# Performance work log

Hardware: AMD Instinct MI355X
Metric: run time of the kernel (lower is better)

## Reference

```python
import jax, jax.numpy as jnp
import numpy as np

EMB = 64   # embedding_dim
OUT = 64   # out_channels (== EMB so conv layers stack)
EF = 16    # num_edge_features
L = 2      # num_layers
NC, NT = 5000, 10000
E, EL = 50000, 20000


def setup_inputs():
    key = jax.random.key(0)
    it = iter(jax.random.split(key, 40))
    def nrm(shape, s=0.05):
        return jax.random.normal(next(it), shape, dtype=jnp.float32) * s
    def ri(n, hi):
        return jax.random.randint(next(it), (n,), 0, hi, dtype=jnp.int32)
    return dict(
        x_c=jnp.arange(NC, dtype=jnp.int32),
        x_t=jnp.arange(NT, dtype=jnp.int32),
        edge_src_ct=ri(E, NC), edge_dst_ct=ri(E, NT),
        edge_src_tc=ri(E, NT), edge_dst_tc=ri(E, NC),
        edge_label_src=ri(EL, NC), edge_label_dst=ri(EL, NT),
        edge_attr_ct=nrm((E, EF), 1.0),
        edge_attr_tc=nrm((E, EF), 1.0),
        edge_label_attr=nrm((EL, EF), 1.0),
        emb_c=nrm((NC, EMB), 1.0), emb_t=nrm((NT, EMB), 1.0),
        ntl_c_w=nrm((EMB, EMB)), ntl_c_b=nrm((EMB,)),
        ntl_t_w=nrm((EMB, EMB)), ntl_t_b=nrm((EMB,)),
        conv_mlp1_w=nrm((L, 2, EF, OUT)), conv_mlp1_b=nrm((L, 2, OUT)),
        conv_mlp2_w=nrm((L, 2, OUT, EMB * OUT)), conv_mlp2_b=nrm((L, 2, EMB * OUT)),
        conv_root_w=nrm((L, 2, EMB, OUT)), conv_root_b=nrm((L, 2, OUT)),
        ph_w0=nrm((2 * EMB + EF, 64)), ph_b0=nrm((64,)),
        ph_w1=nrm((64, 64)), ph_b1=nrm((64,)),
        ph_w2=nrm((64, 1)), ph_b2=nrm((1,)),
    )


def _nnconv(h_src, h_dst, src, dst, eattr, m1w, m1b, m2w, m2b, rw, rb, n_dst):
    # edge-conditioned weight matrices: [E, EMB, OUT]
    W = (jax.nn.relu(eattr @ m1w + m1b) @ m2w + m2b).reshape(-1, EMB, OUT)
    msg = jnp.einsum('ei,eio->eo', h_src[src], W)        # gather + per-edge matmul
    agg = jax.ops.segment_max(msg, dst, num_segments=n_dst)
    agg = jnp.where(jnp.isneginf(agg), 0.0, agg)         # isolated nodes -> 0 (PyG semantics)
    return agg + h_dst @ rw + rb                          # root weight + bias


def reference(x_c, x_t, edge_src_ct, edge_dst_ct, edge_src_tc, edge_dst_tc,
              edge_label_src, edge_label_dst, edge_attr_ct, edge_attr_tc,
              edge_label_attr, emb_c, emb_t, ntl_c_w, ntl_c_b, ntl_t_w, ntl_t_b,
              conv_mlp1_w, conv_mlp1_b, conv_mlp2_w, conv_mlp2_b,
              conv_root_w, conv_root_b, ph_w0, ph_b0, ph_w1, ph_b1, ph_w2, ph_b2):
    h_c = emb_c[x_c] @ ntl_c_w + ntl_c_b
    h_t = emb_t[x_t] @ ntl_t_w + ntl_t_b
    for l in range(L):
        new_t = _nnconv(h_c, h_t, edge_src_ct, edge_dst_ct, edge_attr_ct,
                        conv_mlp1_w[l, 0], conv_mlp1_b[l, 0], conv_mlp2_w[l, 0],
                        conv_mlp2_b[l, 0], conv_root_w[l, 0], conv_root_b[l, 0], NT)
        new_c = _nnconv(h_t, h_c, edge_src_tc, edge_dst_tc, edge_attr_tc,
                        conv_mlp1_w[l, 1], conv_mlp1_b[l, 1], conv_mlp2_w[l, 1],
                        conv_mlp2_b[l, 1], conv_root_w[l, 1], conv_root_b[l, 1], NC)
        h_c, h_t = jax.nn.relu(new_c), jax.nn.relu(new_t)
    z = jnp.concatenate([h_c[edge_label_src], h_t[edge_label_dst], edge_label_attr], axis=-1)
    z = jax.nn.relu(z @ ph_w0 + ph_b0)
    z = jax.nn.relu(z @ ph_w1 + ph_b1)
    logits = z @ ph_w2 + ph_b2
    preds = jax.nn.sigmoid(logits).squeeze()
    return preds, logits
```

## Files before the change

### kernel.cpp

```cpp
#include <hip/hip_runtime.h>
#include <hip/hip_bf16.h>
#include <math.h>

#define NCN   5000
#define NTN   10000
#define NEDGE 50000
#define NLBL  20000
#define EBLK  196

typedef _Float16 f16x8 __attribute__((ext_vector_type(8)));
typedef _Float16 f16x4 __attribute__((ext_vector_type(4)));
typedef float    f32x4 __attribute__((ext_vector_type(4)));

#define HSTRIDE 264
#define NSLICE  130
#define ZSTR    72

__device__ __forceinline__ void atomicMaxF(float* addr, float v) {
  if (v >= 0.0f) atomicMax((int*)addr, __float_as_int(v));
  else           atomicMin((unsigned int*)addr, __float_as_uint(v));
}

__device__ __forceinline__ void stage16(const _Float16* g, _Float16* l) {
  __builtin_amdgcn_global_load_lds(
      (const __attribute__((address_space(1))) void*)g,
      (__attribute__((address_space(3))) void*)l, 16, 0, 0);
}

__global__ __launch_bounds__(256) void fill_neginf(float* __restrict__ p, int n) {
  int i = blockIdx.x * 256 + threadIdx.x;
  if (i < n) p[i] = -INFINITY;
}

__global__ __launch_bounds__(256) void prep_B(
    const float* __restrict__ m2w, const float* __restrict__ m2b,
    _Float16* __restrict__ out)
{
  int p = blockIdx.x / NSLICE;
  int s = blockIdx.x % NSLICE;
  int t = threadIdx.x;
  int hi = t >> 6, col = t & 63;
  const float* w  = m2w + p * 64 * 4096;
  const float* bb = m2b + p * 4096;
  f16x8 v;
  #pragma unroll
  for (int j = 0; j < 8; ++j) {
    float x;
    if (s < 128) {
      int h = s >> 1, i = (s & 1) * 32 + hi * 8 + j;
      x = w[h * 4096 + i * 64 + col];
    } else {
      int i = (s - 128) * 32 + hi * 8 + j;
      x = bb[i * 64 + col];
    }
    v[j] = (_Float16)x;
  }
  *(f16x8*)(out + ((size_t)(p * NSLICE + s)) * 2048 + t * 8) = v;
}

__global__ __launch_bounds__(256) void prep_m1(
    const float* __restrict__ m1w, const float* __restrict__ m1b,
    _Float16* __restrict__ out)
{
  int p = blockIdx.x;
  int t = threadIdx.x;
  int hi = t >> 6, col = t & 63;
  f16x8 v;
  #pragma unroll
  for (int j = 0; j < 8; ++j) {
    int i = hi * 8 + j;
    float x = (i < 16) ? m1w[p * 1024 + i * 64 + col]
            : (i == 16) ? m1b[p * 64 + col] : 0.0f;
    v[j] = (_Float16)x;
  }
  *(f16x8*)(out + (size_t)p * 2048 + t * 8) = v;
}

__global__ __launch_bounds__(256) void prep_headB(
    const float* __restrict__ w0, const float* __restrict__ b0,
    const float* __restrict__ w1, const float* __restrict__ b1,
    _Float16* __restrict__ out)
{
  int s = blockIdx.x;
  int t = threadIdx.x;
  int hi = t >> 6, col = t & 63;
  f16x8 v;
  #pragma unroll
  for (int j = 0; j < 8; ++j) {
    int k = hi * 8 + j;
    float x = 0.0f;
    if (s < 5) {
      int kr = s * 32 + k;
      x = (kr < 144) ? w0[kr * 64 + col] : (kr == 144 ? b0[col] : 0.0f);
    } else {
      int kr = (s - 5) * 32 + k;
      x = (kr < 64) ? w1[kr * 64 + col] : (kr == 64 ? b1[col] : 0.0f);
    }
    v[j] = (_Float16)x;
  }
  *(f16x8*)(out + (size_t)s * 2048 + t * 8) = v;
}

struct NtArgs {
  const float* emb0; const int* idx0; const float* w0; const float* b0; float* out0; int n0; int blk0;
  const float* emb1; const int* idx1; const float* w1; const float* b1; float* out1; int n1;
};

__global__ __launch_bounds__(256) void node_transform2(NtArgs a) {
  int bid = blockIdx.x;
  int dir = (bid >= a.blk0) ? 1 : 0;
  int lb  = bid - (dir ? a.blk0 : 0);
  const float* emb = dir ? a.emb1 : a.emb0;
  const int*   idx = dir ? a.idx1 : a.idx0;
  const float* w   = dir ? a.w1   : a.w0;
  const float* b   = dir ? a.b1   : a.b0;
  float*       out = dir ? a.out1 : a.out0;
  int          n   = dir ? a.n1   : a.n0;

  __shared__ float s_w[64 * 64];
  __shared__ float s_b[64];
  int tid = threadIdx.x;
  for (int i = tid; i < 4096; i += 256) s_w[i] = w[i];
  if (tid < 64) s_b[tid] = b[tid];
  __syncthreads();
  int wave = tid >> 6, lane = tid & 63;
  int node = lb * 4 + wave;
  if (node >= n) return;
  float v = emb[idx[node] * 64 + lane];
  float acc = s_b[lane];
  #pragma unroll 8
  for (int i = 0; i < 64; ++i)
    acc = fmaf(__shfl(v, i, 64), s_w[i * 64 + lane], acc);
  out[node * 64 + lane] = acc;
}

struct ConvArgs {
  const float* h_src0; const int* esrc0; const int* edst0; const float* ea0;
  const _Float16* B0; const _Float16* m10; float* agg0;
  const float* h_src1; const int* esrc1; const int* edst1; const float* ea1;
  const _Float16* B1; const _Float16* m11; float* agg1;
};

__global__ __launch_bounds__(256) void conv_msg_mfma2(ConvArgs a) {
  __shared__ __align__(16) _Float16 s_B[2][4][2048];
  __shared__ __align__(16) _Float16 s_m1f[2048];
  __shared__ __align__(16) _Float16 s_hidT[64 * HSTRIDE];
  __shared__ int s_srcn[256];
  __shared__ int s_dst[256];

  const int bid = blockIdx.x;
  const int dir = (bid >= EBLK) ? 1 : 0;
  const int eb  = bid - (dir ? EBLK : 0);

  const float*    h_src  = dir ? a.h_src1 : a.h_src0;
  const int*      esrc   = dir ? a.esrc1  : a.esrc0;
  const int*      edst   = dir ? a.edst1  : a.edst0;
  const float*    eattr  = dir ? a.ea1    : a.ea0;
  const _Float16* Bready = dir ? a.B1     : a.B0;
  const _Float16* m1rdy  = dir ? a.m11    : a.m10;
  float*          agg    = dir ? a.agg1   : a.agg0;

  const int tid  = threadIdx.x;
  const int e0   = eb * 256;
  const int w    = tid >> 6;
  const int lane = tid & 63;
  const int l15  = lane & 15;
  const int hi   = lane >> 4;
  const int w64  = w * 64;

  stage16(m1rdy + tid * 8, &s_m1f[tid * 8]);
  #pragma unroll
  for (int q = 0; q < 4; ++q)
    stage16(Bready + (size_t)q * 2048 + tid * 8, &s_B[0][q][tid * 8]);

  {
    int ge = e0 + tid;
    s_srcn[tid] = (ge < NEDGE) ? esrc[ge] : 0;
    s_dst[tid]  = (ge < NEDGE) ? edst[ge] : -1;
  }
  __syncthreads();

  f16x8 hv0[4], hv1[4];
  #pragma unroll
  for (int m = 0; m < 4; ++m) {
    int el = w64 + m * 16 + l15;
    const float* src = h_src + (size_t)s_srcn[el] * 64;
    float4 a0 = *(const float4*)(src + hi * 8);
    float4 a1 = *(const float4*)(src + hi * 8 + 4);
    float4 b0 = *(const float4*)(src + 32 + hi * 8);
    float4 b1 = *(const float4*)(src + 32 + hi * 8 + 4);
    hv0[m] = (f16x8){(_Float16)a0.x,(_Float16)a0.y,(_Float16)a0.z,(_Float16)a0.w,
                     (_Float16)a1.x,(_Float16)a1.y,(_Float16)a1.z,(_Float16)a1.w};
    hv1[m] = (f16x8){(_Float16)b0.x,(_Float16)b0.y,(_Float16)b0.z,(_Float16)b0.w,
                     (_Float16)b1.x,(_Float16)b1.y,(_Float16)b1.z,(_Float16)b1.w};
  }

  {
    f16x8 ea[4];
    #pragma unroll
    for (int m = 0; m < 4; ++m) {
      int ge = e0 + w64 + m * 16 + l15;
      f16x8 v = {};
      if (hi < 2) {
        if (ge < NEDGE) {
          float4 f0 = *(const float4*)(eattr + (size_t)ge * 16 + hi * 8);
          float4 f1 = *(const float4*)(eattr + (size_t)ge * 16 + hi * 8 + 4);
          v = (f16x8){(_Float16)f0.x,(_Float16)f0.y,(_Float16)f0.z,(_Float16)f0.w,
                      (_Float16)f1.x,(_Float16)f1.y,(_Float16)f1.z,(_Float16)f1.w};
        }
      } else if (hi == 2) {
        v[0] = (_Float16)1.0f;
      }
      ea[m] = v;
    }
    f32x4 hacc[4][4] = {};
    #pragma unroll
    for (int n = 0; n < 4; ++n) {
      f16x8 bm = *(const f16x8*)&s_m1f[(hi * 64 + n * 16 + l15) * 8];
      #pragma unroll
      for (int m = 0; m < 4; ++m)
        hacc[m][n] = __builtin_amdgcn_mfma_f32_16x16x32_f16(ea[m], bm, hacc[m][n], 0, 0, 0);
    }
    #pragma unroll
    for (int m = 0; m < 4; ++m) {
      #pragma unroll
      for (int n = 0; n < 4; ++n) {
        int h  = n * 16 + l15;
        int e4 = w64 + m * 16 + hi * 4;
        f16x4 hval;
        #pragma unroll
        for (int r = 0; r < 4; ++r) hval[r] = (_Float16)fmaxf(hacc[m][n][r], 0.0f);
        *(f16x4*)&s_hidT[h * HSTRIDE + e4] = hval;
      }
    }
  }

  f32x4 acc[4][4] = {};

#define MFMA_SLICE(P_, SS, HV, HH)                                            \
  {                                                                           \
    f16x8 b0 = *(const f16x8*)&s_B[P_][SS][(hi * 64 +  0 + l15) * 8];         \
    f16x8 b1 = *(const f16x8*)&s_B[P_][SS][(hi * 64 + 16 + l15) * 8];         \
    f16x8 b2 = *(const f16x8*)&s_B[P_][SS][(hi * 64 + 32 + l15) * 8];         \
    f16x8 b3 = *(const f16x8*)&s_B[P_][SS][(hi * 64 + 48 + l15) * 8];         \
    _Pragma("unroll")                                                         \
    for (int m = 0; m < 4; ++m) {                                             \
      f16x8 av = (f16x8)(HV[m] * HH[m]);                                      \
      acc[m][0] = __builtin_amdgcn_mfma_f32_16x16x32_f16(av, b0, acc[m][0], 0, 0, 0); \
      acc[m][1] = __builtin_amdgcn_mfma_f32_16x16x32_f16(av, b1, acc[m][1], 0, 0, 0); \
      acc[m][2] = __builtin_amdgcn_mfma_f32_16x16x32_f16(av, b2, acc[m][2], 0, 0, 0); \
      acc[m][3] = __builtin_amdgcn_mfma_f32_16x16x32_f16(av, b3, acc[m][3], 0, 0, 0); \
    }                                                                         \
  }

#define BIAS_SLICE(P_, SS, HV)                                                \
  {                                                                           \
    f16x8 b0 = *(const f16x8*)&s_B[P_][SS][(hi * 64 +  0 + l15) * 8];         \
    f16x8 b1 = *(const f16x8*)&s_B[P_][SS][(hi * 64 + 16 + l15) * 8];         \
    f16x8 b2 = *(const f16x8*)&s_B[P_][SS][(hi * 64 + 32 + l15) * 8];         \
    f16x8 b3 = *(const f16x8*)&s_B[P_][SS][(hi * 64 + 48 + l15) * 8];         \
    _Pragma("unroll")                                                         \
    for (int m = 0; m < 4; ++m) {                                             \
      f16x8 av = HV[m];                                                       \
      acc[m][0] = __builtin_amdgcn_mfma_f32_16x16x32_f16(av, b0, acc[m][0], 0, 0, 0); \
      acc[m][1] = __builtin_amdgcn_mfma_f32_16x16x32_f16(av, b1, acc[m][1], 0, 0, 0); \
      acc[m][2] = __builtin_amdgcn_mfma_f32_16x16x32_f16(av, b2, acc[m][2], 0, 0, 0); \
      acc[m][3] = __builtin_amdgcn_mfma_f32_16x16x32_f16(av, b3, acc[m][3], 0, 0, 0); \
    }                                                                         \
  }

  for (int p = 0; p < 33; ++p) {
    const int P = p & 1;
    if (p < 31) {
      #pragma unroll
      for (int q = 0; q < 4; ++q)
        stage16(Bready + (size_t)(4 * p + 4 + q) * 2048 + tid * 8,
                &s_B[P ^ 1][q][tid * 8]);
    } else if (p == 31) {
      stage16(Bready + (size_t)128 * 2048 + tid * 8, &s_B[P ^ 1][0][tid * 8]);
      stage16(Bready + (size_t)129 * 2048 + tid * 8, &s_B[P ^ 1][1][tid * 8]);
    }
    if (p < 32) {
      _Float16 hA[4], hB[4];
      #pragma unroll
      for (int m = 0; m < 4; ++m)
        hA[m] = s_hidT[(2 * p) * HSTRIDE + w64 + m * 16 + l15];
      #pragma unroll
      for (int m = 0; m < 4; ++m)
        hB[m] = s_hidT[(2 * p + 1) * HSTRIDE + w64 + m * 16 + l15];
      MFMA_SLICE(P, 0, hv0, hA);
      MFMA_SLICE(P, 1, hv1, hA);
      MFMA_SLICE(P, 2, hv0, hB);
      MFMA_SLICE(P, 3, hv1, hB);
    } else {
      BIAS_SLICE(P, 0, hv0);
      BIAS_SLICE(P, 1, hv1);
    }
    asm volatile("s_waitcnt vmcnt(0)" ::: "memory");
    __builtin_amdgcn_s_barrier();
  }
#undef MFMA_SLICE
#undef BIAS_SLICE

  #pragma unroll
  for (int m = 0; m < 4; ++m) {
    int d0 = s_dst[w64 + m * 16 + hi * 4 + 0];
    int d1 = s_dst[w64 + m * 16 + hi * 4 + 1];
    int d2 = s_dst[w64 + m * 16 + hi * 4 + 2];
    int d3 = s_dst[w64 + m * 16 + hi * 4 + 3];
    #pragma unroll
    for (int n = 0; n < 4; ++n) {
      int o = n * 16 + l15;
      if (d0 >= 0) atomicMaxF(&agg[(size_t)d0 * 64 + o], acc[m][n][0]);
      if (d1 >= 0) atomicMaxF(&agg[(size_t)d1 * 64 + o], acc[m][n][1]);
      if (d2 >= 0) atomicMaxF(&agg[(size_t)d2 * 64 + o], acc[m][n][2]);
      if (d3 >= 0) atomicMaxF(&agg[(size_t)d3 * 64 + o], acc[m][n][3]);
    }
  }
}

struct FinArgs {
  float* agg0; const float* hold0; const float* rw0; const float* rb0; float* hnew0; int n0; int blk0;
  float* agg1; const float* hold1; const float* rw1; const float* rb1; float* hnew1; int n1;
};

__global__ __launch_bounds__(256) void conv_finalize2(FinArgs a) {
  int bid = blockIdx.x;
  int dir = (bid >= a.blk0) ? 1 : 0;
  int lb  = bid - (dir ? a.blk0 : 0);
  float*       agg  = dir ? a.agg1  : a.agg0;
  const float* hold = dir ? a.hold1 : a.hold0;
  const float* rw   = dir ? a.rw1   : a.rw0;
  const float* rb   = dir ? a.rb1   : a.rb0;
  float*       hnew = dir ? a.hnew1 : a.hnew0;
  int          n    = dir ? a.n1    : a.n0;

  __shared__ float s_w[64 * 64];
  __shared__ float s_b[64];
  int tid = threadIdx.x;
  for (int i = tid; i < 4096; i += 256) s_w[i] = rw[i];
  if (tid < 64) s_b[tid] = rb[tid];
  __syncthreads();
  int wave = tid >> 6, lane = tid & 63;
  int node = lb * 4 + wave;
  if (node >= n) return;
  float v = hold[node * 64 + lane];
  float acc = s_b[lane];
  #pragma unroll 8
  for (int i = 0; i < 64; ++i)
    acc = fmaf(__shfl(v, i, 64), s_w[i * 64 + lane], acc);
  float va = agg[node * 64 + lane];
  agg[node * 64 + lane] = -INFINITY;
  if (va == -INFINITY) va = 0.0f;
  hnew[node * 64 + lane] = fmaxf(va + acc, 0.0f);
}

__global__ __launch_bounds__(256) void head_mfma(
    const float* __restrict__ h_c, const float* __restrict__ h_t,
    const int* __restrict__ lsrc, const int* __restrict__ ldst,
    const float* __restrict__ lattr,
    const _Float16* __restrict__ headB,
    const float* __restrict__ w2, const float* __restrict__ b2,
    float* __restrict__ preds, float* __restrict__ logits, int nL)
{
  __shared__ __align__(16) _Float16 s_W[8][2048];
  __shared__ __align__(16) _Float16 s_z[4][32][ZSTR];
  __shared__ float s_w2[64];

  const int tid = threadIdx.x;
  const int wv = tid >> 6, lane = tid & 63;
  const int l15 = lane & 15, hi = lane >> 4;

  #pragma unroll
  for (int s = 0; s < 8; ++s)
    stage16(headB + s * 2048 + tid * 8, &s_W[s][tid * 8]);
  if (tid < 64) s_w2[tid] = w2[tid];
  const float b2v = b2[0];

  const int e0 = blockIdx.x * 128 + wv * 32;

  f16x8 ac[2][2], at[2][2], aa[2];
  #pragma unroll
  for (int m = 0; m < 2; ++m) {
    int e = e0 + m * 16 + l15;
    int ee = (e < nL) ? e : 0;
    const float* pc = h_c + (size_t)lsrc[ee] * 64;
    const float* pt = h_t + (size_t)ldst[ee] * 64;
    #pragma unroll
    for (int half = 0; half < 2; ++half) {
      float4 c0 = *(const float4*)(pc + half * 32 + hi * 8);
      float4 c1 = *(const float4*)(pc + half * 32 + hi * 8 + 4);
      float4 t0 = *(const float4*)(pt + half * 32 + hi * 8);
      float4 t1 = *(const float4*)(pt + half * 32 + hi * 8 + 4);
      ac[m][half] = (f16x8){(_Float16)c0.x,(_Float16)c0.y,(_Float16)c0.z,(_Float16)c0.w,
                            (_Float16)c1.x,(_Float16)c1.y,(_Float16)c1.z,(_Float16)c1.w};
      at[m][half] = (f16x8){(_Float16)t0.x,(_Float16)t0.y,(_Float16)t0.z,(_Float16)t0.w,
                            (_Float16)t1.x,(_Float16)t1.y,(_Float16)t1.z,(_Float16)t1.w};
    }
    f16x8 v = {};
    if (hi < 2) {
      float4 f0 = *(const float4*)(lattr + (size_t)ee * 16 + hi * 8);
      float4 f1 = *(const float4*)(lattr + (size_t)ee * 16 + hi * 8 + 4);
      v = (f16x8){(_Float16)f0.x,(_Float16)f0.y,(_Float16)f0.z,(_Float16)f0.w,
                  (_Float16)f1.x,(_Float16)f1.y,(_Float16)f1.z,(_Float16)f1.w};
    } else if (hi == 2) {
      v[0] = (_Float16)1.0f;
    }
    aa[m] = v;
  }

  __syncthreads();

  f32x4 acc1[2][4] = {};
  #pragma unroll
  for (int s = 0; s < 5; ++s) {
    f16x8 bfr[4];
    #pragma unroll
    for (int nn = 0; nn < 4; ++nn)
      bfr[nn] = *(const f16x8*)&s_W[s][(hi * 64 + nn * 16 + l15) * 8];
    #pragma unroll
    for (int m = 0; m < 2; ++m) {
      f16x8 a = (s == 0) ? ac[m][0] : (s == 1) ? ac[m][1]
              : (s == 2) ? at[m][0] : (s == 3) ? at[m][1] : aa[m];
      #pragma unroll
      for (int nn = 0; nn < 4; ++nn)
        acc1[m][nn] = __builtin_amdgcn_mfma_f32_16x16x32_f16(a, bfr[nn], acc1[m][nn], 0, 0, 0);
    }
  }

  #pragma unroll
  for (int m = 0; m < 2; ++m)
    #pragma unroll
    for (int nn = 0; nn < 4; ++nn)
      #pragma unroll
      for (int r = 0; r < 4; ++r)
        s_z[wv][m * 16 + hi * 4 + r][nn * 16 + l15] =
            (_Float16)fmaxf(acc1[m][nn][r], 0.0f);

  f16x8 abias = {};
  if (hi == 0) abias[0] = (_Float16)1.0f;
  f32x4 acc2[2][4] = {};
  #pragma unroll
  for (int s = 0; s < 3; ++s) {
    f16x8 bfr[4];
    #pragma unroll
    for (int nn = 0; nn < 4; ++nn)
      bfr[nn] = *(const f16x8*)&s_W[5 + s][(hi * 64 + nn * 16 + l15) * 8];
    #pragma unroll
    for (int m = 0; m < 2; ++m) {
      f16x8 a = (s < 2) ? *(const f16x8*)&s_z[wv][m * 16 + l15][s * 32 + hi * 8] : abias;
      #pragma unroll
      for (int nn = 0; nn < 4; ++nn)
        acc2[m][nn] = __builtin_amdgcn_mfma_f32_16x16x32_f16(a, bfr[nn], acc2[m][nn], 0, 0, 0);
    }
  }

  #pragma unroll
  for (int m = 0; m < 2; ++m) {
    float part[4];
    #pragma unroll
    for (int r = 0; r < 4; ++r) {
      float p = 0.0f;
      #pragma unroll
      for (int nn = 0; nn < 4; ++nn)
        p = fmaf(fmaxf(acc2[m][nn][r], 0.0f), s_w2[nn * 16 + l15], p);
      part[r] = p;
    }
    #pragma unroll
    for (int off = 1; off < 16; off <<= 1) {
      #pragma unroll
      for (int r = 0; r < 4; ++r)
        part[r] += __shfl_xor(part[r], off, 64);
    }
    if (l15 == 0) {
      #pragma unroll
      for (int r = 0; r < 4; ++r) {
        int e = e0 + m * 16 + hi * 4 + r;
        if (e < nL) {
          float lg = part[r] + b2v;
          logits[e] = lg;
          preds[e]  = 1.0f / (1.0f + expf(-lg));
        }
      }
    }
  }
}

extern "C" void kernel_launch(void* const* d_in, const int* in_sizes, int n_in,
                              void* d_out, int out_size, void* d_ws, size_t ws_size,
                              hipStream_t stream) {
  const int*   x_c      = (const int*)  d_in[0];
  const int*   x_t      = (const int*)  d_in[1];
  const int*   esrc_ct  = (const int*)  d_in[2];
  const int*   edst_ct  = (const int*)  d_in[3];
  const int*   esrc_tc  = (const int*)  d_in[4];
  const int*   edst_tc  = (const int*)  d_in[5];
  const int*   lbl_src  = (const int*)  d_in[6];
  const int*   lbl_dst  = (const int*)  d_in[7];
  const float* eattr_ct = (const float*)d_in[8];
  const float* eattr_tc = (const float*)d_in[9];
  const float* lbl_attr = (const float*)d_in[10];
  const float* emb_c    = (const float*)d_in[11];
  const float* emb_t    = (const float*)d_in[12];
  const float* ntl_c_w  = (const float*)d_in[13];
  const float* ntl_c_b  = (const float*)d_in[14];
  const float* ntl_t_w  = (const float*)d_in[15];
  const float* ntl_t_b  = (const float*)d_in[16];
  const float* m1w      = (const float*)d_in[17];
  const float* m1b      = (const float*)d_in[18];
  const float* m2w      = (const float*)d_in[19];
  const float* m2b      = (const float*)d_in[20];
  const float* rw       = (const float*)d_in[21];
  const float* rb       = (const float*)d_in[22];
  const float* ph_w0    = (const float*)d_in[23];
  const float* ph_b0    = (const float*)d_in[24];
  const float* ph_w1    = (const float*)d_in[25];
  const float* ph_b1    = (const float*)d_in[26];
  const float* ph_w2    = (const float*)d_in[27];
  const float* ph_b2    = (const float*)d_in[28];

  float* out = (float*)d_out;

  float* ws = (float*)d_ws;
  float* h_c0  = ws;
  float* h_c1  = h_c0 + NCN * 64;
  float* h_t0  = h_c1 + NCN * 64;
  float* h_t1  = h_t0 + NTN * 64;
  float* agg_c = h_t1 + NTN * 64;
  float* agg_t = agg_c + NCN * 64;
  _Float16* Bready  = (_Float16*)(agg_t + NTN * 64);
  _Float16* m1ready = Bready + 4 * NSLICE * 2048;
  _Float16* headBr  = m1ready + 4 * 2048;

  prep_B    <<<4 * NSLICE, 256, 0, stream>>>(m2w, m2b, Bready);
  prep_m1   <<<4, 256, 0, stream>>>(m1w, m1b, m1ready);
  prep_headB<<<8, 256, 0, stream>>>(ph_w0, ph_b0, ph_w1, ph_b1, headBr);

  {
    NtArgs na;
    na.emb0 = emb_c; na.idx0 = x_c; na.w0 = ntl_c_w; na.b0 = ntl_c_b; na.out0 = h_c0; na.n0 = NCN;
    na.blk0 = (NCN + 3) / 4;
    na.emb1 = emb_t; na.idx1 = x_t; na.w1 = ntl_t_w; na.b1 = ntl_t_b; na.out1 = h_t0; na.n1 = NTN;
    node_transform2<<<(NCN + 3) / 4 + (NTN + 3) / 4, 256, 0, stream>>>(na);
  }

  fill_neginf<<<((NCN + NTN) * 64 + 255) / 256, 256, 0, stream>>>(agg_c, (NCN + NTN) * 64);

  float* hc_cur = h_c0; float* hc_nxt = h_c1;
  float* ht_cur = h_t0; float* ht_nxt = h_t1;

  for (int l = 0; l < 2; ++l) {
    int p0 = l * 2 + 0;
    int p1 = l * 2 + 1;
    {
      ConvArgs ca;
      ca.h_src0 = hc_cur; ca.esrc0 = esrc_ct; ca.edst0 = edst_ct; ca.ea0 = eattr_ct;
      ca.B0 = Bready + (size_t)p0 * NSLICE * 2048; ca.m10 = m1ready + (size_t)p0 * 2048;
      ca.agg0 = agg_t;
      ca.h_src1 = ht_cur; ca.esrc1 = esrc_tc; ca.edst1 = edst_tc; ca.ea1 = eattr_tc;
      ca.B1 = Bready + (size_t)p1 * NSLICE * 2048; ca.m11 = m1ready + (size_t)p1 * 2048;
      ca.agg1 = agg_c;
      conv_msg_mfma2<<<2 * EBLK, 256, 0, stream>>>(ca);
    }
    {
      FinArgs fa;
      fa.agg0 = agg_t; fa.hold0 = ht_cur; fa.rw0 = rw + p0 * 4096; fa.rb0 = rb + p0 * 64;
      fa.hnew0 = ht_nxt; fa.n0 = NTN; fa.blk0 = (NTN + 3) / 4;
      fa.agg1 = agg_c; fa.hold1 = hc_cur; fa.rw1 = rw + p1 * 4096; fa.rb1 = rb + p1 * 64;
      fa.hnew1 = hc_nxt; fa.n1 = NCN;
      conv_finalize2<<<(NTN + 3) / 4 + (NCN + 3) / 4, 256, 0, stream>>>(fa);
    }
    float* t;
    t = hc_cur; hc_cur = hc_nxt; hc_nxt = t;
    t = ht_cur; ht_cur = ht_nxt; ht_nxt = t;
  }

  head_mfma<<<(NLBL + 127) / 128, 256, 0, stream>>>(
      hc_cur, ht_cur, lbl_src, lbl_dst, lbl_attr,
      headBr, ph_w2, ph_b2,
      out, out + NLBL, NLBL);
}
```

Measured before the change: 249.6 us.

## Replace atomic segment-max with CSR-sorted edges and deterministic segment reduction

Builds a per-destination CSR (count, scan, scatter) each call, processes edges in destination-sorted order, writes per-edge messages to a dense buffer, and computes the segment max in the finalize kernel instead of with float atomics. This removes 64 scattered atomics per edge and the -inf fill kernel. In exchange it adds three preprocessing kernels, a memset, a single-block scan per direction, and a large message write and read-back through memory (about 25 MB per layer). Padding slots past 50000 read perm entries zeroed by the memset, so they gather edge 0 and write unused rows.

```diff
diff --git a/kernel.cpp b/kernel.cpp
--- a/kernel.cpp
+++ b/kernel.cpp
@@ -5,6 +5,7 @@
 #define NCN   5000
 #define NTN   10000
 #define NEDGE 50000
+#define ESLOT 50176
 #define NLBL  20000
 #define EBLK  196
 
@@ -15,21 +16,11 @@
 #define HSTRIDE 264
 #define NSLICE  130
 #define ZSTR    72
-
-__device__ __forceinline__ void atomicMaxF(float* addr, float v) {
-  if (v >= 0.0f) atomicMax((int*)addr, __float_as_int(v));
-  else           atomicMin((unsigned int*)addr, __float_as_uint(v));
-}
 
 __device__ __forceinline__ void stage16(const _Float16* g, _Float16* l) {
   __builtin_amdgcn_global_load_lds(
       (const __attribute__((address_space(1))) void*)g,
       (__attribute__((address_space(3))) void*)l, 16, 0, 0);
-}
-
-__global__ __launch_bounds__(256) void fill_neginf(float* __restrict__ p, int n) {
-  int i = blockIdx.x * 256 + threadIdx.x;
-  if (i < n) p[i] = -INFINITY;
 }
 
 __global__ __launch_bounds__(256) void prep_B(
@@ -99,6 +90,65 @@
     v[j] = (_Float16)x;
   }
   *(f16x8*)(out + (size_t)s * 2048 + t * 8) = v;
+}
+
+__global__ __launch_bounds__(256) void count_edges(
+    const int* __restrict__ dT, const int* __restrict__ dC,
+    int* __restrict__ cT, int* __restrict__ cC)
+{
+  int i = blockIdx.x * 256 + threadIdx.x;
+  if (i < NEDGE) atomicAdd(&cT[dT[i]], 1);
+  else { int j = i - NEDGE; if (j < NEDGE) atomicAdd(&cC[dC[j]], 1); }
+}
+
+struct ScanArgs { const int* c0; int* o0; int n0; const int* c1; int* o1; int n1; };
+
+__global__ __launch_bounds__(1024) void scan2(ScanArgs a) {
+  const int* c = blockIdx.x ? a.c1 : a.c0;
+  int*       o = blockIdx.x ? a.o1 : a.o0;
+  int        n = blockIdx.x ? a.n1 : a.n0;
+  __shared__ int lds[1024];
+  int t = threadIdx.x;
+  int CH = (n + 1023) / 1024;
+  int base = t * CH;
+  int s = 0;
+  for (int i = 0; i < CH; ++i) { int idx = base + i; if (idx < n) s += c[idx]; }
+  lds[t] = s;
+  __syncthreads();
+  #pragma unroll
+  for (int d = 1; d < 1024; d <<= 1) {
+    int v = (t >= d) ? lds[t - d] : 0;
+    __syncthreads();
+    lds[t] += v;
+    __syncthreads();
+  }
+  int run = lds[t] - s;
+  for (int i = 0; i < CH; ++i) {
+    int idx = base + i;
+    if (idx < n) { o[idx] = run; run += c[idx]; }
+  }
+  if (t == 1023) o[n] = lds[1023];
+}
+
+__global__ __launch_bounds__(256) void scatter_edges(
+    const int* __restrict__ dT, const int* __restrict__ dC,
+    const int* __restrict__ oT, const int* __restrict__ oC,
+    int* __restrict__ curT, int* __restrict__ curC,
+    int* __restrict__ permT, int* __restrict__ permC)
+{
+  int i = blockIdx.x * 256 + threadIdx.x;
+  if (i < NEDGE) {
+    int d = dT[i];
+    int p = atomicAdd(&curT[d], 1);
+    permT[oT[d] + p] = i;
+  } else {
+    int j = i - NEDGE;
+    if (j < NEDGE) {
+      int d = dC[j];
+      int p = atomicAdd(&curC[d], 1);
+      permC[oC[d] + p] = j;
+    }
+  }
 }
 
 struct NtArgs {
@@ -135,10 +185,10 @@
 }
 
 struct ConvArgs {
-  const float* h_src0; const int* esrc0; const int* edst0; const float* ea0;
-  const _Float16* B0; const _Float16* m10; float* agg0;
-  const float* h_src1; const int* esrc1; const int* edst1; const float* ea1;
-  const _Float16* B1; const _Float16* m11; float* agg1;
+  const float* h_src0; const int* esrc0; const float* ea0;
+  const int* perm0; const _Float16* B0; const _Float16* m10; float* msg0;
+  const float* h_src1; const int* esrc1; const float* ea1;
+  const int* perm1; const _Float16* B1; const _Float16* m11; float* msg1;
 };
 
 __global__ __launch_bounds__(256) void conv_msg_mfma2(ConvArgs a) {
@@ -146,7 +196,7 @@
   __shared__ __align__(16) _Float16 s_m1f[2048];
   __shared__ __align__(16) _Float16 s_hidT[64 * HSTRIDE];
   __shared__ int s_srcn[256];
-  __shared__ int s_dst[256];
+  __shared__ int s_eidx[256];
 
   const int bid = blockIdx.x;
   const int dir = (bid >= EBLK) ? 1 : 0;
@@ -154,11 +204,11 @@
 
   const float*    h_src  = dir ? a.h_src1 : a.h_src0;
   const int*      esrc   = dir ? a.esrc1  : a.esrc0;
-  const int*      edst   = dir ? a.edst1  : a.edst0;
   const float*    eattr  = dir ? a.ea1    : a.ea0;
+  const int*      eperm  = dir ? a.perm1  : a.perm0;
   const _Float16* Bready = dir ? a.B1     : a.B0;
   const _Float16* m1rdy  = dir ? a.m11    : a.m10;
-  float*          agg    = dir ? a.agg1   : a.agg0;
+  float*          msg    = dir ? a.msg1   : a.msg0;
 
   const int tid  = threadIdx.x;
   const int e0   = eb * 256;
@@ -174,9 +224,9 @@
     stage16(Bready + (size_t)q * 2048 + tid * 8, &s_B[0][q][tid * 8]);
 
   {
-    int ge = e0 + tid;
-    s_srcn[tid] = (ge < NEDGE) ? esrc[ge] : 0;
-    s_dst[tid]  = (ge < NEDGE) ? edst[ge] : -1;
+    int e = eperm[e0 + tid];
+    s_eidx[tid] = e;
+    s_srcn[tid] = esrc[e];
   }
   __syncthreads();
 
@@ -199,15 +249,14 @@
     f16x8 ea[4];
     #pragma unroll
     for (int m = 0; m < 4; ++m) {
-      int ge = e0 + w64 + m * 16 + l15;
+      int li = w64 + m * 16 + l15;
+      int e  = s_eidx[li];
       f16x8 v = {};
       if (hi < 2) {
-        if (ge < NEDGE) {
-          float4 f0 = *(const float4*)(eattr + (size_t)ge * 16 + hi * 8);
-          float4 f1 = *(const float4*)(eattr + (size_t)ge * 16 + hi * 8 + 4);
-          v = (f16x8){(_Float16)f0.x,(_Float16)f0.y,(_Float16)f0.z,(_Float16)f0.w,
-                      (_Float16)f1.x,(_Float16)f1.y,(_Float16)f1.z,(_Float16)f1.w};
-        }
+        float4 f0 = *(const float4*)(eattr + (size_t)e * 16 + hi * 8);
+        float4 f1 = *(const float4*)(eattr + (size_t)e * 16 + hi * 8 + 4);
+        v = (f16x8){(_Float16)f0.x,(_Float16)f0.y,(_Float16)f0.z,(_Float16)f0.w,
+                    (_Float16)f1.x,(_Float16)f1.y,(_Float16)f1.z,(_Float16)f1.w};
       } else if (hi == 2) {
         v[0] = (_Float16)1.0f;
       }
@@ -304,31 +353,30 @@
 
   #pragma unroll
   for (int m = 0; m < 4; ++m) {
-    int d0 = s_dst[w64 + m * 16 + hi * 4 + 0];
-    int d1 = s_dst[w64 + m * 16 + hi * 4 + 1];
-    int d2 = s_dst[w64 + m * 16 + hi * 4 + 2];
-    int d3 = s_dst[w64 + m * 16 + hi * 4 + 3];
-    #pragma unroll
-    for (int n = 0; n < 4; ++n) {
-      int o = n * 16 + l15;
-      if (d0 >= 0) atomicMaxF(&agg[(size_t)d0 * 64 + o], acc[m][n][0]);
-      if (d1 >= 0) atomicMaxF(&agg[(size_t)d1 * 64 + o], acc[m][n][1]);
-      if (d2 >= 0) atomicMaxF(&agg[(size_t)d2 * 64 + o], acc[m][n][2]);
-      if (d3 >= 0) atomicMaxF(&agg[(size_t)d3 * 64 + o], acc[m][n][3]);
-    }
-  }
-}
-
-struct FinArgs {
-  float* agg0; const float* hold0; const float* rw0; const float* rb0; float* hnew0; int n0; int blk0;
-  float* agg1; const float* hold1; const float* rw1; const float* rb1; float* hnew1; int n1;
+    #pragma unroll
+    for (int r = 0; r < 4; ++r) {
+      int sl = e0 + w64 + m * 16 + hi * 4 + r;
+      float* row = msg + (size_t)sl * 64;
+      #pragma unroll
+      for (int n = 0; n < 4; ++n)
+        row[n * 16 + l15] = acc[m][n][r];
+    }
+  }
+}
+
+struct SegArgs {
+  const float* msg0; const int* off0; const float* hold0; const float* rw0; const float* rb0;
+  float* hnew0; int n0; int blk0;
+  const float* msg1; const int* off1; const float* hold1; const float* rw1; const float* rb1;
+  float* hnew1; int n1;
 };
 
-__global__ __launch_bounds__(256) void conv_finalize2(FinArgs a) {
+__global__ __launch_bounds__(256) void segfin2(SegArgs a) {
   int bid = blockIdx.x;
   int dir = (bid >= a.blk0) ? 1 : 0;
   int lb  = bid - (dir ? a.blk0 : 0);
-  float*       agg  = dir ? a.agg1  : a.agg0;
+  const float* msg  = dir ? a.msg1  : a.msg0;
+  const int*   off  = dir ? a.off1  : a.off0;
   const float* hold = dir ? a.hold1 : a.hold0;
   const float* rw   = dir ? a.rw1   : a.rw0;
   const float* rb   = dir ? a.rb1   : a.rb0;
@@ -344,15 +392,19 @@
   int wave = tid >> 6, lane = tid & 63;
   int node = lb * 4 + wave;
   if (node >= n) return;
+
+  int k0 = off[node], k1 = off[node + 1];
+  float mx = -INFINITY;
+  for (int k = k0; k < k1; ++k)
+    mx = fmaxf(mx, msg[(size_t)k * 64 + lane]);
+  if (k0 == k1) mx = 0.0f;
+
   float v = hold[node * 64 + lane];
   float acc = s_b[lane];
   #pragma unroll 8
   for (int i = 0; i < 64; ++i)
     acc = fmaf(__shfl(v, i, 64), s_w[i * 64 + lane], acc);
-  float va = agg[node * 64 + lane];
-  agg[node * 64 + lane] = -INFINITY;
-  if (va == -INFINITY) va = 0.0f;
-  hnew[node * 64 + lane] = fmaxf(va + acc, 0.0f);
+  hnew[node * 64 + lane] = fmaxf(mx + acc, 0.0f);
 }
 
 __global__ __launch_bounds__(256) void head_mfma(
@@ -522,15 +574,35 @@
   float* out = (float*)d_out;
 
   float* ws = (float*)d_ws;
-  float* h_c0  = ws;
-  float* h_c1  = h_c0 + NCN * 64;
-  float* h_t0  = h_c1 + NCN * 64;
-  float* h_t1  = h_t0 + NTN * 64;
-  float* agg_c = h_t1 + NTN * 64;
-  float* agg_t = agg_c + NCN * 64;
-  _Float16* Bready  = (_Float16*)(agg_t + NTN * 64);
+  float* h_c0 = ws;
+  float* h_c1 = h_c0 + NCN * 64;
+  float* h_t0 = h_c1 + NCN * 64;
+  float* h_t1 = h_t0 + NTN * 64;
+  float* msgT = h_t1 + NTN * 64;
+  float* msgC = msgT + (size_t)ESLOT * 64;
+  _Float16* Bready  = (_Float16*)(msgC + (size_t)ESLOT * 64);
   _Float16* m1ready = Bready + 4 * NSLICE * 2048;
   _Float16* headBr  = m1ready + 4 * 2048;
+  int* ip     = (int*)(headBr + 8 * 2048);
+  int* offT   = ip;               ip += NTN + 1;
+  int* offC   = ip;               ip += NCN + 1;
+  int* cntT   = ip;               ip += NTN;
+  int* cntC   = ip;               ip += NCN;
+  int* curT   = ip;               ip += NTN;
+  int* curC   = ip;               ip += NCN;
+  int* permT  = ip;               ip += ESLOT;
+  int* permC  = ip;               ip += ESLOT;
+  size_t zero_bytes = (size_t)(2 * (NTN + NCN) + 2 * ESLOT) * sizeof(int);
+
+  hipMemsetAsync(cntT, 0, zero_bytes, stream);
+  count_edges<<<(2 * NEDGE + 255) / 256, 256, 0, stream>>>(edst_ct, edst_tc, cntT, cntC);
+  {
+    ScanArgs sa; sa.c0 = cntT; sa.o0 = offT; sa.n0 = NTN;
+    sa.c1 = cntC; sa.o1 = offC; sa.n1 = NCN;
+    scan2<<<2, 1024, 0, stream>>>(sa);
+  }
+  scatter_edges<<<(2 * NEDGE + 255) / 256, 256, 0, stream>>>(
+      edst_ct, edst_tc, offT, offC, curT, curC, permT, permC);
 
   prep_B    <<<4 * NSLICE, 256, 0, stream>>>(m2w, m2b, Bready);
   prep_m1   <<<4, 256, 0, stream>>>(m1w, m1b, m1ready);
@@ -544,8 +616,6 @@
     node_transform2<<<(NCN + 3) / 4 + (NTN + 3) / 4, 256, 0, stream>>>(na);
   }
 
-  fill_neginf<<<((NCN + NTN) * 64 + 255) / 256, 256, 0, stream>>>(agg_c, (NCN + NTN) * 64);
-
   float* hc_cur = h_c0; float* hc_nxt = h_c1;
   float* ht_cur = h_t0; float* ht_nxt = h_t1;
 
@@ -554,21 +624,23 @@
     int p1 = l * 2 + 1;
     {
       ConvArgs ca;
-      ca.h_src0 = hc_cur; ca.esrc0 = esrc_ct; ca.edst0 = edst_ct; ca.ea0 = eattr_ct;
+      ca.h_src0 = hc_cur; ca.esrc0 = esrc_ct; ca.ea0 = eattr_ct; ca.perm0 = permT;
       ca.B0 = Bready + (size_t)p0 * NSLICE * 2048; ca.m10 = m1ready + (size_t)p0 * 2048;
-      ca.agg0 = agg_t;
-      ca.h_src1 = ht_cur; ca.esrc1 = esrc_tc; ca.edst1 = edst_tc; ca.ea1 = eattr_tc;
+      ca.msg0 = msgT;
+      ca.h_src1 = ht_cur; ca.esrc1 = esrc_tc; ca.ea1 = eattr_tc; ca.perm1 = permC;
       ca.B1 = Bready + (size_t)p1 * NSLICE * 2048; ca.m11 = m1ready + (size_t)p1 * 2048;
-      ca.agg1 = agg_c;
+      ca.msg1 = msgC;
       conv_msg_mfma2<<<2 * EBLK, 256, 0, stream>>>(ca);
     }
     {
-      FinArgs fa;
-      fa.agg0 = agg_t; fa.hold0 = ht_cur; fa.rw0 = rw + p0 * 4096; fa.rb0 = rb + p0 * 64;
-      fa.hnew0 = ht_nxt; fa.n0 = NTN; fa.blk0 = (NTN + 3) / 4;
-      fa.agg1 = agg_c; fa.hold1 = hc_cur; fa.rw1 = rw + p1 * 4096; fa.rb1 = rb + p1 * 64;
-      fa.hnew1 = hc_nxt; fa.n1 = NCN;
-      conv_finalize2<<<(NTN + 3) / 4 + (NCN + 3) / 4, 256, 0, stream>>>(fa);
+      SegArgs sg;
+      sg.msg0 = msgT; sg.off0 = offT; sg.hold0 = ht_cur;
+      sg.rw0 = rw + p0 * 4096; sg.rb0 = rb + p0 * 64; sg.hnew0 = ht_nxt;
+      sg.n0 = NTN; sg.blk0 = (NTN + 3) / 4;
+      sg.msg1 = msgC; sg.off1 = offC; sg.hold1 = hc_cur;
+      sg.rw1 = rw + p1 * 4096; sg.rb1 = rb + p1 * 64; sg.hnew1 = hc_nxt;
+      sg.n1 = NCN;
+      segfin2<<<(NTN + 3) / 4 + (NCN + 3) / 4, 256, 0, stream>>>(sg);
     }
     float* t;
     t = hc_cur; hc_cur = hc_nxt; hc_nxt = t;
```

New measurement: 236.8 us. -5.1%, faster.
